# Kernel tuning notes

Hardware: AMD Instinct MI355X
Metric: run time of the kernel (lower is better)

Reference implementation:

```python
import jax, jax.numpy as jnp
import numpy as np

K = 3          # deformable kernel size
N = K * K      # sampling points per output pixel
PAD = 1
BN_EPS = 1e-5


def setup_inputs() -> dict:
    key = jax.random.key(0)
    ks = jax.random.split(key, 6)
    B, C, H, W = 32, 103, 32, 32
    Cout = 32
    x = jax.random.normal(ks[0], (B, C, H, W), jnp.float32)
    # offset-predicting conv: 2*N output channels (N y-offsets then N x-offsets)
    w_off = jax.random.normal(ks[1], (2 * N, C, K, K), jnp.float32) * 0.01
    b_off = jnp.zeros((2 * N,), jnp.float32)
    # main deformable conv weight
    w = jax.random.normal(ks[2], (Cout, C, K, K), jnp.float32) * (1.0 / np.sqrt(C * N))
    b = jnp.zeros((Cout,), jnp.float32)
    # BatchNorm (eval mode) params
    gamma = jax.random.uniform(ks[3], (Cout,), jnp.float32, 0.5, 1.5)
    beta = jax.random.normal(ks[4], (Cout,), jnp.float32) * 0.1
    run_mean = jax.random.normal(ks[5], (Cout,), jnp.float32) * 0.1
    run_var = jnp.ones((Cout,), jnp.float32)
    return {"x": x, "w_off": w_off, "b_off": b_off, "w": w, "b": b,
            "gamma": gamma, "beta": beta, "run_mean": run_mean, "run_var": run_var}


def _deform_conv(x, w_off, b_off, w, b):
    B, C, H, W = x.shape
    # predicted offsets: (B, 2N, H, W) -> (B, H, W, N) each for y and x
    off = jax.lax.conv_general_dilated(x, w_off, (1, 1), [(PAD, PAD), (PAD, PAD)])
    off = off + b_off[None, :, None, None]
    off_y = jnp.transpose(off[:, :N], (0, 2, 3, 1))
    off_x = jnp.transpose(off[:, N:], (0, 2, 3, 1))
    # regular kernel grid offsets p_n in {-1,0,1}^2
    ky, kx = jnp.meshgrid(jnp.arange(-1, 2, dtype=jnp.float32),
                          jnp.arange(-1, 2, dtype=jnp.float32), indexing='ij')
    kn_y, kn_x = ky.reshape(-1), kx.reshape(-1)  # (N,)
    # base grid p_0 in padded coordinates (stride 1, padding 1 -> starts at 1)
    p0_y = jnp.arange(1, H + 1, dtype=jnp.float32)[None, :, None, None]
    p0_x = jnp.arange(1, W + 1, dtype=jnp.float32)[None, None, :, None]
    Hp, Wp = H + 2 * PAD, W + 2 * PAD
    py = jnp.clip(p0_y + kn_y + off_y, 0.0, Hp - 1.0)  # (B,H,W,N)
    px = jnp.clip(p0_x + kn_x + off_x, 0.0, Wp - 1.0)
    # zero-padded input, flattened spatial for gather
    xp = jnp.pad(x, ((0, 0), (0, 0), (PAD, PAD), (PAD, PAD)))
    xf = xp.reshape(B, C, Hp * Wp)
    y0 = jnp.clip(jnp.floor(py).astype(jnp.int32), 0, Hp - 2)
    x0 = jnp.clip(jnp.floor(px).astype(jnp.int32), 0, Wp - 2)
    y1, x1 = y0 + 1, x0 + 1
    wy = (py - y0.astype(py.dtype))[:, None]  # (B,1,H,W,N)
    wx = (px - x0.astype(px.dtype))[:, None]

    def gather(yi, xi):
        idx = (yi * Wp + xi).reshape(B, -1)                      # (B, H*W*N)
        g = jnp.take_along_axis(xf, idx[:, None, :], axis=2)    # (B, C, H*W*N)
        return g.reshape(B, C, H, W, N)

    v00, v01 = gather(y0, x0), gather(y0, x1)
    v10, v11 = gather(y1, x0), gather(y1, x1)
    samp = (v00 * (1 - wy) * (1 - wx) + v01 * (1 - wy) * wx
            + v10 * wy * (1 - wx) + v11 * wy * wx)               # (B,C,H,W,N)
    out = jnp.einsum('bchwn,ocn->bohw', samp, w.reshape(w.shape[0], C, N))
    return out + b[None, :, None, None]


def reference(x, w_off, b_off, w, b, gamma, beta, run_mean, run_var):
    out = _deform_conv(x, w_off, b_off, w, b)
    # BatchNorm2d (eval mode) + ReLU
    inv = gamma * jax.lax.rsqrt(run_var + BN_EPS)
    out = out * inv[None, :, None, None] + (beta - run_mean * inv)[None, :, None, None]
    return jax.nn.relu(out)
```

## Files before the change

kernel.cpp:

```cpp
#include <hip/hip_runtime.h>


#define CC    103
#define COUT  32
#define KSC   5
#define RSU   34
#define PLSU  1158
#define NPAIR 8
#define BUF_U (NPAIR * PLSU)

typedef __attribute__((ext_vector_type(8))) _Float16 f16x8;
typedef __attribute__((ext_vector_type(2))) _Float16 h2;
typedef __attribute__((ext_vector_type(2))) __fp16  fp16x2;
typedef __attribute__((ext_vector_type(4))) float f32x4;

#define WTPM_W 0
#define WTPO_W 17920
#define BN_W   35840

__global__ void k_prep(const float* __restrict__ w, const float* __restrict__ w_off,
                       const float* __restrict__ bias, const float* __restrict__ gamma,
                       const float* __restrict__ beta, const float* __restrict__ mean,
                       const float* __restrict__ var,
                       unsigned short* __restrict__ wtpm, unsigned short* __restrict__ wtpo,
                       float* __restrict__ bn) {
    int tid = blockIdx.x * 256 + threadIdx.x;
    if (tid < 71680) {
        int half_ = tid >= 35840 ? 1 : 0;
        int e = tid - half_ * 35840;
        const float* src = half_ ? w_off : w;
        unsigned short* dst = half_ ? wtpo : wtpm;
        int mrows = half_ ? 18 : 32;
        int j = e & 7, lane = (e >> 3) & 63, tile = e >> 9;
        int mt = tile & 1, chs = tile >> 1;
        int s = chs % 5, ch = chs / 5;
        int o = mt * 16 + (lane & 15);
        int kl = s * 32 + (lane >> 4) * 8 + j;
        int n = kl >> 4, c = ch * 16 + (kl & 15);
        float v = 0.f;
        if (n < 9 && c < CC && o < mrows) v = src[o * (CC * 9) + c * 9 + n];
        union { _Float16 h; unsigned short u; } cv;
        cv.h = (_Float16)v;
        dst[e] = cv.u;
    }
    if (tid < 32) {
        float inv = gamma[tid] * rsqrtf(var[tid] + 1e-5f);
        bn[tid]      = inv;
        bn[32 + tid] = beta[tid] + (bias[tid] - mean[tid]) * inv;
    }
}

__global__ void __launch_bounds__(512, 4)
k_fused(const float* __restrict__ x, const float* __restrict__ b_off,
        const unsigned short* __restrict__ wtpo, const unsigned short* __restrict__ wtpm,
        const float* __restrict__ bn, float* __restrict__ out) {
    __shared__ unsigned int ldsp[2 * BUF_U];
    __shared__ float exch[18 * 64];

    int bid = blockIdx.x;
    int b   = (bid & 7) * 4 + ((bid >> 3) & 3);
    int pxg = bid >> 5;

    int t = threadIdx.x, lane = t & 63, wv = t >> 6;
    int kh = wv >> 2;
    int pw = wv & 3;
    int pxl = pw * 16 + (lane & 15);
    int px  = pxg * 64 + pxl;
    int h = px >> 5, wq = px & 31;
    int kg = lane >> 4;
    int hi = kg >> 1;
    int pb = (kg & 1) * 4;

    unsigned int* mybuf = ldsp + kh * BUF_U;

    for (int i = t; i < 2 * BUF_U; i += 512) ldsp[i] = 0u;

    const float* xb = x + b * (CC * 1024);
    int tl = t & 255;
    int sr = tl >> 3, sk = (tl & 7) * 4;

    const int KYL[5] = {0,0,1,2,2}, KXL[5] = {0,2,1,0,2};
    const int KYH[5] = {0,1,1,2,2}, KXH[5] = {1,0,2,1,2};
    const int TAPL[5] = {0,2,4,6,8}, TAPH[5] = {1,3,5,7,8};
    int myky[5], mykx[5], mytap[5];
#pragma unroll
    for (int s = 0; s < 5; s++) {
        myky[s] = hi ? KYH[s] : KYL[s];
        mykx[s] = hi ? KXH[s] : KXL[s];
        mytap[s] = hi ? TAPH[s] : TAPL[s];
    }

    auto stage = [&](int ch) {
        const float* srcb = xb + sr * 32 + sk;
        unsigned int* dstb = mybuf + (sr + 1) * RSU + 2 + sk;
#pragma unroll
        for (int i = 0; i < NPAIR; i++) {
            int c = ch * 16 + 2 * i;
            if (c < CC) {
                float4 a = *(const float4*)(srcb + c * 1024);
                float4 bb = make_float4(0.f, 0.f, 0.f, 0.f);
                if (c + 1 < CC) bb = *(const float4*)(srcb + (c + 1) * 1024);
                union { fp16x2 h; unsigned u; } p0, p1, p2, p3;
                p0.h = __builtin_amdgcn_cvt_pkrtz(a.x, bb.x);
                p1.h = __builtin_amdgcn_cvt_pkrtz(a.y, bb.y);
                p2.h = __builtin_amdgcn_cvt_pkrtz(a.z, bb.z);
                p3.h = __builtin_amdgcn_cvt_pkrtz(a.w, bb.w);
                *(uint2*)(dstb + i * PLSU)     = make_uint2(p0.u, p1.u);
                *(uint2*)(dstb + i * PLSU + 2) = make_uint2(p2.u, p3.u);
            }
        }
    };

    f32x4 acc0 = {0.f, 0.f, 0.f, 0.f};
    f32x4 acc1 = {0.f, 0.f, 0.f, 0.f};

#pragma unroll
    for (int it = 0; it < 4; it++) {
        const int ch = kh ? (2 * it) : (it < 3 ? 2 * it + 1 : -1);
        __syncthreads();
        if (ch >= 0) stage(ch);
        __syncthreads();
        if (ch >= 0) {
            const unsigned short* wch = wtpo + ch * 5120;
#pragma unroll
            for (int s = 0; s < KSC; s++) {
                const unsigned int* cell = mybuf + pb * PLSU
                                         + (h + myky[s]) * RSU + 1 + (wq + mykx[s]);
                union { unsigned u[4]; f16x8 v; } bu;
#pragma unroll
                for (int jj = 0; jj < 4; jj++) bu.u[jj] = cell[jj * PLSU];
                f16x8 a0 = *(const f16x8*)(wch + s * 1024 + lane * 8);
                f16x8 a1 = *(const f16x8*)(wch + s * 1024 + 512 + lane * 8);
                acc0 = __builtin_amdgcn_mfma_f32_16x16x32_f16(a0, bu.v, acc0, 0, 0, 0);
                acc1 = __builtin_amdgcn_mfma_f32_16x16x32_f16(a1, bu.v, acc1, 0, 0, 0);
            }
        }
    }

    __syncthreads();
    if (kh == 0) {
        float* ex = exch + pxl;
#pragma unroll
        for (int reg = 0; reg < 4; reg++) ex[(kg * 4 + reg) * 64] = acc0[reg];
        if (kg == 0) { ex[16 * 64] = acc1[0]; ex[17 * 64] = acc1[1]; }
    }
    __syncthreads();
    if (kh == 1) {
        float* ex = exch + pxl;
#pragma unroll
        for (int reg = 0; reg < 4; reg++) ex[(kg * 4 + reg) * 64] += acc0[reg];
        if (kg == 0) { ex[16 * 64] += acc1[0]; ex[17 * 64] += acc1[1]; }
    }
    __syncthreads();

    int cofs[KSC];
    h2  W[KSC][4];
#pragma unroll
    for (int s = 0; s < KSC; s++) {
        int tap = mytap[s];
        float oy = exch[tap * 64 + pxl] + b_off[tap];
        float ox = exch[(9 + tap) * 64 + pxl] + b_off[9 + tap];
        float py  = (float)(h + myky[s]) + oy;
        float pxx = (float)(wq + mykx[s]) + ox;
        py  = fminf(fmaxf(py, 0.f), 33.f);
        pxx = fminf(fmaxf(pxx, 0.f), 33.f);
        int y0 = min((int)py, 32);
        int x0 = min((int)pxx, 32);
        float fy = py - (float)y0;
        float fx = pxx - (float)x0;
        float w00 = (1.f - fy) * (1.f - fx), w01 = (1.f - fy) * fx;
        float w10 = fy * (1.f - fx),          w11 = fy * fx;
        W[s][0] = (h2){(_Float16)w00, (_Float16)w00};
        W[s][1] = (h2){(_Float16)w01, (_Float16)w01};
        W[s][2] = (h2){(_Float16)w10, (_Float16)w10};
        W[s][3] = (h2){(_Float16)w11, (_Float16)w11};
        cofs[s] = pb * PLSU + y0 * RSU + 1 + x0;
    }

    acc0 = (f32x4){0.f, 0.f, 0.f, 0.f};
    acc1 = (f32x4){0.f, 0.f, 0.f, 0.f};
#pragma unroll
    for (int it = 0; it < 4; it++) {
        const int ch = kh ? (6 - 2 * it) : (it < 3 ? 5 - 2 * it : -1);
        if (it > 0) {
            __syncthreads();
            if (ch >= 0) stage(ch);
            else {
                float* ex2 = (float*)ldsp;
                float* e = ex2 + pxl;
#pragma unroll
                for (int reg = 0; reg < 4; reg++) {
                    e[(kg * 4 + reg) * 64]        = acc0[reg];
                    e[(16 + kg * 4 + reg) * 64]   = acc1[reg];
                }
            }
            __syncthreads();
        }
        if (ch >= 0) {
            const unsigned short* wch = wtpm + ch * 5120;
#pragma unroll
            for (int s = 0; s < KSC; s++) {
                const unsigned int* cell = mybuf + cofs[s];
                union { unsigned u[4]; f16x8 v; } bu;
#pragma unroll
                for (int jj = 0; jj < 4; jj++) {
                    union { unsigned u; h2 hh; } t0, t1, b0, b1;
                    t0.u = cell[jj * PLSU];
                    t1.u = cell[jj * PLSU + 1];
                    b0.u = cell[jj * PLSU + RSU];
                    b1.u = cell[jj * PLSU + RSU + 1];
                    h2 sm = t0.hh * W[s][0] + t1.hh * W[s][1]
                          + b0.hh * W[s][2] + b1.hh * W[s][3];
                    union { h2 hh; unsigned u; } r; r.hh = sm;
                    bu.u[jj] = r.u;
                }
                f16x8 a0 = *(const f16x8*)(wch + s * 1024 + lane * 8);
                f16x8 a1 = *(const f16x8*)(wch + s * 1024 + 512 + lane * 8);
                acc0 = __builtin_amdgcn_mfma_f32_16x16x32_f16(a0, bu.v, acc0, 0, 0, 0);
                acc1 = __builtin_amdgcn_mfma_f32_16x16x32_f16(a1, bu.v, acc1, 0, 0, 0);
            }
        }
    }

    __syncthreads();
    if (kh == 1) {
        const float* ex2 = (const float*)ldsp;
        float* op = out + (size_t)b * COUT * 1024 + px;
#pragma unroll
        for (int mt = 0; mt < 2; mt++) {
            f32x4 a = mt ? acc1 : acc0;
#pragma unroll
            for (int reg = 0; reg < 4; reg++) {
                int o = mt * 16 + kg * 4 + reg;
                float tot = a[reg] + ex2[o * 64 + pxl];
                float v = tot * bn[o] + bn[32 + o];
                op[o * 1024] = fmaxf(v, 0.f);
            }
        }
    }
}

extern "C" void kernel_launch(void* const* d_in, const int* in_sizes, int n_in,
                              void* d_out, int out_size, void* d_ws, size_t ws_size,
                              hipStream_t stream) {
    const float* x      = (const float*)d_in[0];
    const float* w_off  = (const float*)d_in[1];
    const float* b_off  = (const float*)d_in[2];
    const float* w      = (const float*)d_in[3];
    const float* bias   = (const float*)d_in[4];
    const float* gamma  = (const float*)d_in[5];
    const float* beta   = (const float*)d_in[6];
    const float* rmean  = (const float*)d_in[7];
    const float* rvar   = (const float*)d_in[8];
    float* out = (float*)d_out;

    float* ws = (float*)d_ws;
    unsigned short* wtpm = (unsigned short*)(ws + WTPM_W);
    unsigned short* wtpo = (unsigned short*)(ws + WTPO_W);
    float*          bn   = ws + BN_W;

    k_prep <<<280, 256, 0, stream>>>(w, w_off, bias, gamma, beta, rmean, rvar,
                                     wtpm, wtpo, bn);
    k_fused<<<512, 512, 0, stream>>>(x, b_off, wtpo, wtpm, bn, out);
}
```

Before: 108.8 us.

## Prefetch next channel chunk into registers while computing current chunk

Splits staging into a global-load phase and a pack-and-write-to-LDS phase, so the next chunk's global loads are issued before the MFMA work on the current chunk. This hides global memory latency behind compute. The first load is also issued before the LDS zeroing. The LDS plane stride changes, likely to reduce bank conflicts. In exchange, 16 float4 values stay live in registers, which raises register pressure under launch_bounds(512,4). The loops are no longer unrolled.

```diff
diff --git a/kernel.cpp b/kernel.cpp
--- a/kernel.cpp
+++ b/kernel.cpp
@@ -5,7 +5,7 @@
 #define COUT  32
 #define KSC   5
 #define RSU   34
-#define PLSU  1158
+#define PLSU  1164
 #define NPAIR 8
 #define BUF_U (NPAIR * PLSU)
 
@@ -63,8 +63,7 @@
 
     int t = threadIdx.x, lane = t & 63, wv = t >> 6;
     int kh = wv >> 2;
-    int pw = wv & 3;
-    int pxl = pw * 16 + (lane & 15);
+    int pxl = (wv & 3) * 16 + (lane & 15);
     int px  = pxg * 64 + pxl;
     int h = px >> 5, wq = px & 31;
     int kg = lane >> 4;
@@ -73,8 +72,6 @@
 
     unsigned int* mybuf = ldsp + kh * BUF_U;
 
-    for (int i = t; i < 2 * BUF_U; i += 512) ldsp[i] = 0u;
-
     const float* xb = x + b * (CC * 1024);
     int tl = t & 255;
     int sr = tl >> 3, sk = (tl & 7) * 4;
@@ -90,42 +87,58 @@
         mytap[s] = hi ? TAPH[s] : TAPL[s];
     }
 
-    auto stage = [&](int ch) {
-        const float* srcb = xb + sr * 32 + sk;
-        unsigned int* dstb = mybuf + (sr + 1) * RSU + 2 + sk;
+    float4 L[NPAIR], M[NPAIR];
+    auto loadx = [&](int ch) {
+        const float* s0 = xb + sr * 32 + sk;
 #pragma unroll
         for (int i = 0; i < NPAIR; i++) {
             int c = ch * 16 + 2 * i;
             if (c < CC) {
-                float4 a = *(const float4*)(srcb + c * 1024);
-                float4 bb = make_float4(0.f, 0.f, 0.f, 0.f);
-                if (c + 1 < CC) bb = *(const float4*)(srcb + (c + 1) * 1024);
-                union { fp16x2 h; unsigned u; } p0, p1, p2, p3;
-                p0.h = __builtin_amdgcn_cvt_pkrtz(a.x, bb.x);
-                p1.h = __builtin_amdgcn_cvt_pkrtz(a.y, bb.y);
-                p2.h = __builtin_amdgcn_cvt_pkrtz(a.z, bb.z);
-                p3.h = __builtin_amdgcn_cvt_pkrtz(a.w, bb.w);
+                L[i] = *(const float4*)(s0 + c * 1024);
+                if (c + 1 < CC) M[i] = *(const float4*)(s0 + (c + 1) * 1024);
+                else            M[i] = make_float4(0.f, 0.f, 0.f, 0.f);
+            }
+        }
+    };
+    auto packwrite = [&](int ch) {
+        unsigned int* dstb = mybuf + (sr + 1) * RSU + 2 + sk;
+#pragma unroll
+        for (int i = 0; i < NPAIR; i++) {
+            int c = ch * 16 + 2 * i;
+            if (c < CC) {
+                union { fp16x2 hh; unsigned u; } p0, p1, p2, p3;
+                p0.hh = __builtin_amdgcn_cvt_pkrtz(L[i].x, M[i].x);
+                p1.hh = __builtin_amdgcn_cvt_pkrtz(L[i].y, M[i].y);
+                p2.hh = __builtin_amdgcn_cvt_pkrtz(L[i].z, M[i].z);
+                p3.hh = __builtin_amdgcn_cvt_pkrtz(L[i].w, M[i].w);
                 *(uint2*)(dstb + i * PLSU)     = make_uint2(p0.u, p1.u);
                 *(uint2*)(dstb + i * PLSU + 2) = make_uint2(p2.u, p3.u);
             }
         }
     };
 
+    auto chunk1 = [&](int it) { return kh ? (2 * it) : (it < 3 ? 2 * it + 1 : -1); };
+    auto chunk2 = [&](int it) { return kh ? (6 - 2 * it) : (it < 3 ? 5 - 2 * it : -1); };
+
     f32x4 acc0 = {0.f, 0.f, 0.f, 0.f};
     f32x4 acc1 = {0.f, 0.f, 0.f, 0.f};
 
-#pragma unroll
+    loadx(chunk1(0));
+    for (int i = t; i < 2 * BUF_U; i += 512) ldsp[i] = 0u;
+    __syncthreads();
+
     for (int it = 0; it < 4; it++) {
-        const int ch = kh ? (2 * it) : (it < 3 ? 2 * it + 1 : -1);
-        __syncthreads();
-        if (ch >= 0) stage(ch);
-        __syncthreads();
+        int ch = chunk1(it);
+        if (ch >= 0) packwrite(ch);
+        __syncthreads();
+        int nx = (it < 3) ? chunk1(it + 1) : -1;
+        if (nx >= 0) loadx(nx);
         if (ch >= 0) {
             const unsigned short* wch = wtpo + ch * 5120;
 #pragma unroll
             for (int s = 0; s < KSC; s++) {
                 const unsigned int* cell = mybuf + pb * PLSU
-                                         + (h + myky[s]) * RSU + 1 + (wq + mykx[s]);
+                    + (h + myky[s]) * RSU + 1 + (wq + mykx[s]);
                 union { unsigned u[4]; f16x8 v; } bu;
 #pragma unroll
                 for (int jj = 0; jj < 4; jj++) bu.u[jj] = cell[jj * PLSU];
@@ -135,9 +148,9 @@
                 acc1 = __builtin_amdgcn_mfma_f32_16x16x32_f16(a1, bu.v, acc1, 0, 0, 0);
             }
         }
-    }
-
-    __syncthreads();
+        __syncthreads();
+    }
+
     if (kh == 0) {
         float* ex = exch + pxl;
 #pragma unroll
@@ -179,23 +192,22 @@
 
     acc0 = (f32x4){0.f, 0.f, 0.f, 0.f};
     acc1 = (f32x4){0.f, 0.f, 0.f, 0.f};
-#pragma unroll
     for (int it = 0; it < 4; it++) {
-        const int ch = kh ? (6 - 2 * it) : (it < 3 ? 5 - 2 * it : -1);
+        int ch = chunk2(it);
         if (it > 0) {
-            __syncthreads();
-            if (ch >= 0) stage(ch);
+            if (ch >= 0) packwrite(ch);
             else {
-                float* ex2 = (float*)ldsp;
-                float* e = ex2 + pxl;
+                float* e = (float*)ldsp + pxl;
 #pragma unroll
                 for (int reg = 0; reg < 4; reg++) {
-                    e[(kg * 4 + reg) * 64]        = acc0[reg];
-                    e[(16 + kg * 4 + reg) * 64]   = acc1[reg];
+                    e[(kg * 4 + reg) * 64]      = acc0[reg];
+                    e[(16 + kg * 4 + reg) * 64] = acc1[reg];
                 }
             }
-            __syncthreads();
-        }
+        }
+        __syncthreads();
+        int nx = (it < 3) ? chunk2(it + 1) : -1;
+        if (nx >= 0) loadx(nx);
         if (ch >= 0) {
             const unsigned short* wch = wtpm + ch * 5120;
 #pragma unroll
@@ -220,9 +232,9 @@
                 acc1 = __builtin_amdgcn_mfma_f32_16x16x32_f16(a1, bu.v, acc1, 0, 0, 0);
             }
         }
-    }
-
-    __syncthreads();
+        __syncthreads();
+    }
+
     if (kh == 1) {
         const float* ex2 = (const float*)ldsp;
         float* op = out + (size_t)b * COUT * 1024 + px;
```

After: 108.2 us. No clear change (-0.5%).

## Split K-steps across half-blocks sharing one LDS buffer instead of channel chunks

Applied to the files above, without the earlier changes.

The two half-blocks no longer hold separate LDS buffers and split channel chunks between them. Instead a single buffer is staged cooperatively per chunk, and the half-blocks split the 5 K-steps per chunk (3 and 2). This halves LDS use and raises the launch-bound occupancy hint from 4 to 6, aiming for more resident blocks. In exchange there are more barriers, 7 sequential chunk iterations instead of 4, and an uneven 3/2 work split between the two halves. The plane stride is also padded.

```diff
diff --git a/kernel.cpp b/kernel.cpp
--- a/kernel.cpp
+++ b/kernel.cpp
@@ -3,10 +3,10 @@
 
 #define CC    103
 #define COUT  32
-#define KSC   5
 #define RSU   34
-#define PLSU  1158
+#define PLSU  1164
 #define NPAIR 8
+#define NCHUNK 7
 #define BUF_U (NPAIR * PLSU)
 
 typedef __attribute__((ext_vector_type(8))) _Float16 f16x8;
@@ -50,11 +50,11 @@
     }
 }
 
-__global__ void __launch_bounds__(512, 4)
+__global__ void __launch_bounds__(512, 6)
 k_fused(const float* __restrict__ x, const float* __restrict__ b_off,
         const unsigned short* __restrict__ wtpo, const unsigned short* __restrict__ wtpm,
         const float* __restrict__ bn, float* __restrict__ out) {
-    __shared__ unsigned int ldsp[2 * BUF_U];
+    __shared__ unsigned int ldsp[BUF_U];
     __shared__ float exch[18 * 64];
 
     int bid = blockIdx.x;
@@ -63,81 +63,78 @@
 
     int t = threadIdx.x, lane = t & 63, wv = t >> 6;
     int kh = wv >> 2;
-    int pw = wv & 3;
-    int pxl = pw * 16 + (lane & 15);
+    int pxl = (wv & 3) * 16 + (lane & 15);
     int px  = pxg * 64 + pxl;
     int h = px >> 5, wq = px & 31;
     int kg = lane >> 4;
-    int hi = kg >> 1;
+    int hi2 = kg >> 1;
     int pb = (kg & 1) * 4;
-
-    unsigned int* mybuf = ldsp + kh * BUF_U;
-
-    for (int i = t; i < 2 * BUF_U; i += 512) ldsp[i] = 0u;
+    const int ns = kh ? 2 : 3;
+
+    int myky[3], mykx[3], mytap[3];
+#pragma unroll
+    for (int j = 0; j < 3; j++) {
+        int as = kh * 3 + j;
+        int tap = 2 * as + hi2; if (tap > 8) tap = 8;
+        mytap[j] = tap; myky[j] = tap / 3; mykx[j] = tap % 3;
+    }
 
     const float* xb = x + b * (CC * 1024);
-    int tl = t & 255;
-    int sr = tl >> 3, sk = (tl & 7) * 4;
-
-    const int KYL[5] = {0,0,1,2,2}, KXL[5] = {0,2,1,0,2};
-    const int KYH[5] = {0,1,1,2,2}, KXH[5] = {1,0,2,1,2};
-    const int TAPL[5] = {0,2,4,6,8}, TAPH[5] = {1,3,5,7,8};
-    int myky[5], mykx[5], mytap[5];
-#pragma unroll
-    for (int s = 0; s < 5; s++) {
-        myky[s] = hi ? KYH[s] : KYL[s];
-        mykx[s] = hi ? KXH[s] : KXL[s];
-        mytap[s] = hi ? TAPH[s] : TAPL[s];
-    }
+
+    int sp = t >> 6;
+    int srow = (t & 63) >> 1;
+    int shr = (t & 1) * 16;
 
     auto stage = [&](int ch) {
-        const float* srcb = xb + sr * 32 + sk;
-        unsigned int* dstb = mybuf + (sr + 1) * RSU + 2 + sk;
-#pragma unroll
-        for (int i = 0; i < NPAIR; i++) {
-            int c = ch * 16 + 2 * i;
-            if (c < CC) {
-                float4 a = *(const float4*)(srcb + c * 1024);
-                float4 bb = make_float4(0.f, 0.f, 0.f, 0.f);
-                if (c + 1 < CC) bb = *(const float4*)(srcb + (c + 1) * 1024);
-                union { fp16x2 h; unsigned u; } p0, p1, p2, p3;
-                p0.h = __builtin_amdgcn_cvt_pkrtz(a.x, bb.x);
-                p1.h = __builtin_amdgcn_cvt_pkrtz(a.y, bb.y);
-                p2.h = __builtin_amdgcn_cvt_pkrtz(a.z, bb.z);
-                p3.h = __builtin_amdgcn_cvt_pkrtz(a.w, bb.w);
-                *(uint2*)(dstb + i * PLSU)     = make_uint2(p0.u, p1.u);
-                *(uint2*)(dstb + i * PLSU + 2) = make_uint2(p2.u, p3.u);
-            }
+        int c = ch * 16 + 2 * sp;
+        if (c >= CC) return;
+        const float* s0 = xb + c * 1024 + srow * 32 + shr;
+        unsigned int* dst = ldsp + sp * PLSU + (srow + 1) * RSU + 2 + shr;
+        bool hasM = (c + 1 < CC);
+        const float* s1 = s0 + 1024;
+#pragma unroll
+        for (int q = 0; q < 4; q++) {
+            float4 a = *(const float4*)(s0 + 4 * q);
+            float4 m = hasM ? *(const float4*)(s1 + 4 * q)
+                            : make_float4(0.f, 0.f, 0.f, 0.f);
+            union { fp16x2 hh; unsigned u; } p0, p1, p2, p3;
+            p0.hh = __builtin_amdgcn_cvt_pkrtz(a.x, m.x);
+            p1.hh = __builtin_amdgcn_cvt_pkrtz(a.y, m.y);
+            p2.hh = __builtin_amdgcn_cvt_pkrtz(a.z, m.z);
+            p3.hh = __builtin_amdgcn_cvt_pkrtz(a.w, m.w);
+            *(uint2*)(dst + 4 * q)     = make_uint2(p0.u, p1.u);
+            *(uint2*)(dst + 4 * q + 2) = make_uint2(p2.u, p3.u);
         }
     };
 
     f32x4 acc0 = {0.f, 0.f, 0.f, 0.f};
     f32x4 acc1 = {0.f, 0.f, 0.f, 0.f};
 
-#pragma unroll
-    for (int it = 0; it < 4; it++) {
-        const int ch = kh ? (2 * it) : (it < 3 ? 2 * it + 1 : -1);
-        __syncthreads();
-        if (ch >= 0) stage(ch);
-        __syncthreads();
-        if (ch >= 0) {
-            const unsigned short* wch = wtpo + ch * 5120;
-#pragma unroll
-            for (int s = 0; s < KSC; s++) {
-                const unsigned int* cell = mybuf + pb * PLSU
-                                         + (h + myky[s]) * RSU + 1 + (wq + mykx[s]);
+    for (int i = t; i < BUF_U; i += 512) ldsp[i] = 0u;
+    __syncthreads();
+
+    for (int ch = 0; ch < NCHUNK; ch++) {
+        stage(ch);
+        __syncthreads();
+        const unsigned short* wch = wtpo + ch * 5120;
+#pragma unroll
+        for (int j = 0; j < 3; j++) {
+            if (j < ns) {
+                int as = kh * 3 + j;
+                const unsigned int* cell = ldsp + pb * PLSU
+                    + (h + myky[j]) * RSU + 1 + (wq + mykx[j]);
                 union { unsigned u[4]; f16x8 v; } bu;
 #pragma unroll
                 for (int jj = 0; jj < 4; jj++) bu.u[jj] = cell[jj * PLSU];
-                f16x8 a0 = *(const f16x8*)(wch + s * 1024 + lane * 8);
-                f16x8 a1 = *(const f16x8*)(wch + s * 1024 + 512 + lane * 8);
+                f16x8 a0 = *(const f16x8*)(wch + as * 1024 + lane * 8);
+                f16x8 a1 = *(const f16x8*)(wch + as * 1024 + 512 + lane * 8);
                 acc0 = __builtin_amdgcn_mfma_f32_16x16x32_f16(a0, bu.v, acc0, 0, 0, 0);
                 acc1 = __builtin_amdgcn_mfma_f32_16x16x32_f16(a1, bu.v, acc1, 0, 0, 0);
             }
         }
-    }
-
-    __syncthreads();
+        __syncthreads();
+    }
+
     if (kh == 0) {
         float* ex = exch + pxl;
 #pragma unroll
@@ -153,15 +150,15 @@
     }
     __syncthreads();
 
-    int cofs[KSC];
-    h2  W[KSC][4];
-#pragma unroll
-    for (int s = 0; s < KSC; s++) {
-        int tap = mytap[s];
+    int cofs[3];
+    h2  W[3][4];
+#pragma unroll
+    for (int j = 0; j < 3; j++) {
+        int tap = mytap[j];
         float oy = exch[tap * 64 + pxl] + b_off[tap];
         float ox = exch[(9 + tap) * 64 + pxl] + b_off[9 + tap];
-        float py  = (float)(h + myky[s]) + oy;
-        float pxx = (float)(wq + mykx[s]) + ox;
+        float py  = (float)(h + myky[j]) + oy;
+        float pxx = (float)(wq + mykx[j]) + ox;
         py  = fminf(fmaxf(py, 0.f), 33.f);
         pxx = fminf(fmaxf(pxx, 0.f), 33.f);
         int y0 = min((int)py, 32);
@@ -170,37 +167,25 @@
         float fx = pxx - (float)x0;
         float w00 = (1.f - fy) * (1.f - fx), w01 = (1.f - fy) * fx;
         float w10 = fy * (1.f - fx),          w11 = fy * fx;
-        W[s][0] = (h2){(_Float16)w00, (_Float16)w00};
-        W[s][1] = (h2){(_Float16)w01, (_Float16)w01};
-        W[s][2] = (h2){(_Float16)w10, (_Float16)w10};
-        W[s][3] = (h2){(_Float16)w11, (_Float16)w11};
-        cofs[s] = pb * PLSU + y0 * RSU + 1 + x0;
+        W[j][0] = (h2){(_Float16)w00, (_Float16)w00};
+        W[j][1] = (h2){(_Float16)w01, (_Float16)w01};
+        W[j][2] = (h2){(_Float16)w10, (_Float16)w10};
+        W[j][3] = (h2){(_Float16)w11, (_Float16)w11};
+        cofs[j] = pb * PLSU + y0 * RSU + 1 + x0;
     }
 
     acc0 = (f32x4){0.f, 0.f, 0.f, 0.f};
     acc1 = (f32x4){0.f, 0.f, 0.f, 0.f};
-#pragma unroll
-    for (int it = 0; it < 4; it++) {
-        const int ch = kh ? (6 - 2 * it) : (it < 3 ? 5 - 2 * it : -1);
-        if (it > 0) {
-            __syncthreads();
-            if (ch >= 0) stage(ch);
-            else {
-                float* ex2 = (float*)ldsp;
-                float* e = ex2 + pxl;
-#pragma unroll
-                for (int reg = 0; reg < 4; reg++) {
-                    e[(kg * 4 + reg) * 64]        = acc0[reg];
-                    e[(16 + kg * 4 + reg) * 64]   = acc1[reg];
-                }
-            }
-            __syncthreads();
-        }
-        if (ch >= 0) {
-            const unsigned short* wch = wtpm + ch * 5120;
-#pragma unroll
-            for (int s = 0; s < KSC; s++) {
-                const unsigned int* cell = mybuf + cofs[s];
+    for (int it = 0; it < NCHUNK; it++) {
+        int ch = 6 - it;
+        if (it > 0) stage(ch);
+        __syncthreads();
+        const unsigned short* wch = wtpm + ch * 5120;
+#pragma unroll
+        for (int j = 0; j < 3; j++) {
+            if (j < ns) {
+                int as = kh * 3 + j;
+                const unsigned int* cell = ldsp + cofs[j];
                 union { unsigned u[4]; f16x8 v; } bu;
 #pragma unroll
                 for (int jj = 0; jj < 4; jj++) {
@@ -209,22 +194,31 @@
                     t1.u = cell[jj * PLSU + 1];
                     b0.u = cell[jj * PLSU + RSU];
                     b1.u = cell[jj * PLSU + RSU + 1];
-                    h2 sm = t0.hh * W[s][0] + t1.hh * W[s][1]
-                          + b0.hh * W[s][2] + b1.hh * W[s][3];
+                    h2 sm = t0.hh * W[j][0] + t1.hh * W[j][1]
+                          + b0.hh * W[j][2] + b1.hh * W[j][3];
                     union { h2 hh; unsigned u; } r; r.hh = sm;
                     bu.u[jj] = r.u;
                 }
-                f16x8 a0 = *(const f16x8*)(wch + s * 1024 + lane * 8);
-                f16x8 a1 = *(const f16x8*)(wch + s * 1024 + 512 + lane * 8);
+                f16x8 a0 = *(const f16x8*)(wch + as * 1024 + lane * 8);
+                f16x8 a1 = *(const f16x8*)(wch + as * 1024 + 512 + lane * 8);
                 acc0 = __builtin_amdgcn_mfma_f32_16x16x32_f16(a0, bu.v, acc0, 0, 0, 0);
                 acc1 = __builtin_amdgcn_mfma_f32_16x16x32_f16(a1, bu.v, acc1, 0, 0, 0);
             }
         }
-    }
-
+        __syncthreads();
+    }
+
+    float* ex2 = (float*)ldsp;
+    if (kh == 0) {
+        float* e = ex2 + pxl;
+#pragma unroll
+        for (int reg = 0; reg < 4; reg++) {
+            e[(kg * 4 + reg) * 64]      = acc0[reg];
+            e[(16 + kg * 4 + reg) * 64] = acc1[reg];
+        }
+    }
     __syncthreads();
     if (kh == 1) {
-        const float* ex2 = (const float*)ldsp;
         float* op = out + (size_t)b * COUT * 1024 + px;
 #pragma unroll
         for (int mt = 0; mt < 2; mt++) {
```

After: 128.4 us. +18.0%, slower.
